# Kernel tuning notes

Hardware: AMD Instinct MI355X
Metric: run time of the kernel (lower is better)

## Reference

```python
import jax, jax.numpy as jnp
import numpy as np

N_ATOMS = 100000
N_BONDS = 200000
N_MOLS = 4000
ATOMS_PER_MOL = 25
MAX_NB = 6
ATOM_FDIM = 133
BOND_FDIM = 14
HIDDEN = 300
DEPTH = 3


def setup_inputs() -> dict:
    key = jax.random.key(0)
    ks = jax.random.split(key, 8)
    f_atoms = jax.random.normal(ks[0], (N_ATOMS, ATOM_FDIM), dtype=jnp.float32)
    f_bonds = jax.random.normal(ks[1], (N_BONDS, BOND_FDIM), dtype=jnp.float32)
    # incoming-bond lists per atom (irregular gather targets)
    a2b = jax.random.randint(ks[2], (N_ATOMS, MAX_NB), 0, N_BONDS, dtype=jnp.int32)
    # source atom of each directed bond
    b2a = jax.random.randint(ks[3], (N_BONDS,), 0, N_ATOMS, dtype=jnp.int32)
    # reverse bond: directed bonds come in pairs (2i, 2i+1)
    b2revb = (jnp.arange(N_BONDS, dtype=jnp.int32) ^ 1)
    # contiguous [start, size] per molecule
    starts = jnp.arange(N_MOLS, dtype=jnp.int32) * ATOMS_PER_MOL
    sizes = jnp.full((N_MOLS,), ATOMS_PER_MOL, dtype=jnp.int32)
    a_scope = jnp.stack([starts, sizes], axis=1)
    W_i = jax.random.normal(ks[4], (HIDDEN, ATOM_FDIM + BOND_FDIM), dtype=jnp.float32) * 0.05
    W_h = jax.random.normal(ks[5], (HIDDEN, HIDDEN), dtype=jnp.float32) * 0.05
    W_o = jax.random.normal(ks[6], (HIDDEN, ATOM_FDIM + HIDDEN), dtype=jnp.float32) * 0.05
    b_o = jax.random.normal(ks[7], (HIDDEN,), dtype=jnp.float32) * 0.05
    return {"f_atoms": f_atoms, "f_bonds": f_bonds, "a2b": a2b, "b2a": b2a,
            "b2revb": b2revb, "a_scope": a_scope, "W_i": W_i, "W_h": W_h,
            "W_o": W_o, "b_o": b_o}


def reference(f_atoms, f_bonds, a2b, b2a, b2revb, a_scope, W_i, W_h, W_o, b_o):
    # initial directed-bond messages: [f_atoms[src], f_bonds] -> Linear -> ReLU
    input_feats = jnp.concatenate([f_atoms[b2a], f_bonds], axis=1)  # (E, 147)
    message = jax.nn.relu(input_feats @ W_i.T)  # (E, H)
    for _ in range(DEPTH - 1):
        nei_a_message = message[a2b].sum(axis=1)          # (V, H) gather+sum
        nei_message = nei_a_message[b2a] - message[b2revb]  # (E, H)
        message = jax.nn.relu(nei_message @ W_h.T)
    a_message = message[a2b].sum(axis=1)  # (V, H)
    atom_hiddens = jax.nn.relu(jnp.concatenate([f_atoms, a_message], axis=1) @ W_o.T + b_o)
    # vectorized scope mean-pool (scopes are contiguous ranges)
    starts = a_scope[:, 0]
    sizes = a_scope[:, 1]
    seg_ids = jnp.searchsorted(starts, jnp.arange(atom_hiddens.shape[0]), side='right') - 1
    sums = jax.ops.segment_sum(atom_hiddens, seg_ids, num_segments=N_MOLS)
    denom = jnp.maximum(sizes, 1).astype(atom_hiddens.dtype)[:, None]
    mol_vecs = jnp.where((sizes > 0)[:, None], sums / denom, 0.0)
    return mol_vecs
```

## Files before the change

### kernel.cpp

```cpp
#include <hip/hip_runtime.h>
#include <stdint.h>

#define N_ATOMS   100000
#define N_BONDS   200000
#define N_MOLS    4000
#define MAX_NB    6
#define ATOM_FDIM 133
#define BOND_FDIM 14
#define HIDDEN    300
#define NPAD      320

typedef __attribute__((ext_vector_type(8))) short          bf16x8;
typedef __attribute__((ext_vector_type(8))) unsigned short u16x8;
typedef __attribute__((ext_vector_type(4))) float          f32x4;
typedef __attribute__((ext_vector_type(4))) unsigned int   u32x4;

static __device__ __forceinline__ float u2f(unsigned int u) {
  union { unsigned int u; float f; } v; v.u = u; return v.f;
}
static __device__ __forceinline__ unsigned int f2u(float f) {
  union { float f; unsigned int u; } v; v.f = f; return v.u;
}
static __device__ __forceinline__ float bflo(unsigned int u) { return u2f(u << 16); }
static __device__ __forceinline__ float bfhi(unsigned int u) { return u2f(u & 0xffff0000u); }
static __device__ __forceinline__ unsigned short f2bf_rn(float f) {
  unsigned int u = f2u(f);
  return (unsigned short)((u + 0x7fffu + ((u >> 16) & 1u)) >> 16);
}
static __device__ __forceinline__ unsigned int pack_rn(float lo, float hi) {
  return ((unsigned int)f2bf_rn(hi) << 16) | f2bf_rn(lo);
}

__global__ __launch_bounds__(256) void convw_kernel(
    const float* __restrict__ w, unsigned short* __restrict__ o,
    int Ksrc, int seg1, int src2off, int seg2dst, int seg2len, int KP) {
  int total = NPAD * KP;
  for (int idx = blockIdx.x * 256 + threadIdx.x; idx < total; idx += gridDim.x * 256) {
    int n = idx / KP, k = idx - n * KP;
    int src = -1;
    if (k < seg1) src = k;
    else if (k >= seg2dst && k < seg2dst + seg2len) src = src2off + (k - seg2dst);
    float v = (n < HIDDEN && src >= 0) ? w[(size_t)n * Ksrc + src] : 0.f;
    o[idx] = f2bf_rn(v);
  }
}

template<int KP, int MODE, int FS, int FW, bool RELU, bool BIAS>
__global__ __launch_bounds__(256, 2) void gemm_dense(
    const float* __restrict__ Af, const unsigned short* Ab,
    const unsigned short* __restrict__ W, const float* __restrict__ bias,
    unsigned short* out, int M) {
  constexpr int NST = KP / 32;
  __shared__ __align__(16) unsigned short As[NST * 2048];

  const int b0   = blockIdx.x * 64;
  const int tid  = threadIdx.x;
  const int lane = tid & 63;
  const int wave = tid >> 6;
  const int sr   = tid >> 2;
  const int q    = tid & 3;

  int row = b0 + sr;
  if (row >= M) row = M - 1;
  const int dbase = (sr >> 4) * 512 + (q * 16 + (sr & 15)) * 8;

  auto stage_chunk = [&](int ks) -> u16x8 {
    u16x8 r;
    if (MODE == 0) {
      r = *(const u16x8*)(Ab + (size_t)row * KP + ks * 32 + q * 8);
    } else if (MODE == 1) {
#pragma unroll
      for (int j = 0; j < 8; j++) {
        int k = ks * 32 + q * 8 + j;
        float v = (k < FW) ? Af[(size_t)row * FS + k] : 0.f;
        r[j] = f2bf_rn(v);
      }
    } else {
      if (ks < 5) {
#pragma unroll
        for (int j = 0; j < 8; j++) {
          int k = ks * 32 + q * 8 + j;
          float v = (k < ATOM_FDIM) ? Af[(size_t)row * ATOM_FDIM + k] : 0.f;
          r[j] = f2bf_rn(v);
        }
      } else {
        r = *(const u16x8*)(Ab + (size_t)row * NPAD + (ks - 5) * 32 + q * 8);
      }
    }
    return r;
  };

  constexpr int G = (NST < 5) ? NST : 5;
#pragma unroll
  for (int ks0 = 0; ks0 < NST; ks0 += G) {
    u16x8 vals[G];
#pragma unroll
    for (int j = 0; j < G; j++) { int ks = ks0 + j; if (ks < NST) vals[j] = stage_chunk(ks); }
#pragma unroll
    for (int j = 0; j < G; j++) { int ks = ks0 + j; if (ks < NST) *(u16x8*)&As[ks * 2048 + dbase] = vals[j]; }
  }
  __syncthreads();

  f32x4 acc[4][5];
#pragma unroll
  for (int m = 0; m < 4; m++)
#pragma unroll
    for (int n = 0; n < 5; n++) acc[m][n] = (f32x4){0.f, 0.f, 0.f, 0.f};

  const int nbase = wave * 80;
  const int ar = lane & 15, kq = lane >> 4;
  const unsigned short* Wl = W + (size_t)(nbase + ar) * KP + kq * 8;

#pragma unroll
  for (int ks = 0; ks < NST; ks++) {
    bf16x8 af[4];
#pragma unroll
    for (int m = 0; m < 4; m++) af[m] = *(const bf16x8*)&As[ks * 2048 + m * 512 + lane * 8];
#pragma unroll
    for (int nf = 0; nf < 5; nf++) {
      bf16x8 bfr = *(const bf16x8*)(Wl + (size_t)nf * 16 * KP + ks * 32);
#pragma unroll
      for (int m = 0; m < 4; m++)
        acc[m][nf] = __builtin_amdgcn_mfma_f32_16x16x32_bf16(af[m], bfr, acc[m][nf], 0, 0, 0);
    }
  }

#pragma unroll
  for (int m = 0; m < 4; m++) {
#pragma unroll
    for (int rr = 0; rr < 4; rr++) {
      int orow = b0 + m * 16 + (lane >> 4) * 4 + rr;
      if (orow >= M) continue;
#pragma unroll
      for (int nf = 0; nf < 5; nf++) {
        int ocol = nbase + nf * 16 + ar;
        float v = acc[m][nf][rr];
        if (BIAS) v += (ocol < HIDDEN) ? bias[ocol] : 0.f;
        if (RELU) v = v > 0.f ? v : 0.f;
        out[(size_t)orow * NPAD + ocol] = f2bf_rn(v);
      }
    }
  }
}

__global__ __launch_bounds__(256) void agg_kernel(
    const unsigned short* __restrict__ src, const int* __restrict__ a2b,
    unsigned short* __restrict__ dst) {
  const int TPA = NPAD / 16;
  int idx = blockIdx.x * 256 + threadIdx.x;
  if (idx >= N_ATOMS * TPA) return;
  int a  = idx / TPA;
  int kc = (idx - a * TPA) * 16;
  int bidx[MAX_NB];
#pragma unroll
  for (int j = 0; j < MAX_NB; j++) bidx[j] = a2b[a * MAX_NB + j];
  float slo[8], shi[8];
#pragma unroll
  for (int t = 0; t < 8; t++) { slo[t] = 0.f; shi[t] = 0.f; }
#pragma unroll
  for (int j = 0; j < MAX_NB; j++) {
    const u32x4* p = (const u32x4*)(src + (size_t)bidx[j] * NPAD + kc);
    u32x4 v0 = p[0], v1 = p[1];
#pragma unroll
    for (int t = 0; t < 4; t++) {
      slo[t]     += bflo(v0[t]); shi[t]     += bfhi(v0[t]);
      slo[4 + t] += bflo(v1[t]); shi[4 + t] += bfhi(v1[t]);
    }
  }
  u32x4 o0, o1;
#pragma unroll
  for (int t = 0; t < 4; t++) { o0[t] = pack_rn(slo[t], shi[t]); o1[t] = pack_rn(slo[4 + t], shi[4 + t]); }
  u32x4* qp = (u32x4*)(dst + (size_t)a * NPAD + kc);
  qp[0] = o0; qp[1] = o1;
}

__global__ __launch_bounds__(256) void combine0_kernel(
    const unsigned short* __restrict__ PAi, const unsigned short* PBi,
    const int* __restrict__ b2a, unsigned short* msg) {
  const int TPB = NPAD / 16;
  int idx = blockIdx.x * 256 + threadIdx.x;
  if (idx >= N_BONDS * TPB) return;
  int b  = idx / TPB;
  int kc = (idx - b * TPB) * 16;
  int g = b2a[b];
  const u32x4* pa = (const u32x4*)(PAi + (size_t)g * NPAD + kc);
  const u32x4* pb = (const u32x4*)(PBi + (size_t)b * NPAD + kc);
  u32x4 a0 = pa[0], a1 = pa[1], b0 = pb[0], b1 = pb[1];
  u32x4 o0, o1;
#pragma unroll
  for (int t = 0; t < 4; t++) {
    float l0 = bflo(a0[t]) + bflo(b0[t]), h0 = bfhi(a0[t]) + bfhi(b0[t]);
    float l1 = bflo(a1[t]) + bflo(b1[t]), h1 = bfhi(a1[t]) + bfhi(b1[t]);
    l0 = l0 > 0.f ? l0 : 0.f; h0 = h0 > 0.f ? h0 : 0.f;
    l1 = l1 > 0.f ? l1 : 0.f; h1 = h1 > 0.f ? h1 : 0.f;
    o0[t] = pack_rn(l0, h0); o1[t] = pack_rn(l1, h1);
  }
  u32x4* qp = (u32x4*)(msg + (size_t)b * NPAD + kc);
  qp[0] = o0; qp[1] = o1;
}

__global__ __launch_bounds__(256) void combineH_kernel(
    const unsigned short* __restrict__ neiZ, const unsigned short* Zh,
    const int* __restrict__ b2a, unsigned short* msg) {
  const int TPB = NPAD / 16;
  const int NPAIR = N_BONDS / 2;
  int idx = blockIdx.x * 256 + threadIdx.x;
  if (idx >= NPAIR * TPB) return;
  int p  = idx / TPB;
  int kc = (idx - p * TPB) * 16;
  int b0i = 2 * p, b1i = 2 * p + 1;
  int g0 = b2a[b0i], g1 = b2a[b1i];
  const u32x4* pn0 = (const u32x4*)(neiZ + (size_t)g0 * NPAD + kc);
  const u32x4* pn1 = (const u32x4*)(neiZ + (size_t)g1 * NPAD + kc);
  const u32x4* pz0 = (const u32x4*)(Zh + (size_t)b1i * NPAD + kc);
  const u32x4* pz1 = (const u32x4*)(Zh + (size_t)b0i * NPAD + kc);
  u32x4 n00 = pn0[0], n01 = pn0[1], n10 = pn1[0], n11 = pn1[1];
  u32x4 z00 = pz0[0], z01 = pz0[1], z10 = pz1[0], z11 = pz1[1];
  u32x4 o00, o01, o10, o11;
#pragma unroll
  for (int t = 0; t < 4; t++) {
    float a, c;
    a = bflo(n00[t]) - bflo(z00[t]); c = bfhi(n00[t]) - bfhi(z00[t]);
    o00[t] = pack_rn(a > 0.f ? a : 0.f, c > 0.f ? c : 0.f);
    a = bflo(n01[t]) - bflo(z01[t]); c = bfhi(n01[t]) - bfhi(z01[t]);
    o01[t] = pack_rn(a > 0.f ? a : 0.f, c > 0.f ? c : 0.f);
    a = bflo(n10[t]) - bflo(z10[t]); c = bfhi(n10[t]) - bfhi(z10[t]);
    o10[t] = pack_rn(a > 0.f ? a : 0.f, c > 0.f ? c : 0.f);
    a = bflo(n11[t]) - bflo(z11[t]); c = bfhi(n11[t]) - bfhi(z11[t]);
    o11[t] = pack_rn(a > 0.f ? a : 0.f, c > 0.f ? c : 0.f);
  }
  u32x4* q0 = (u32x4*)(msg + (size_t)b0i * NPAD + kc);
  u32x4* q1 = (u32x4*)(msg + (size_t)b1i * NPAD + kc);
  q0[0] = o00; q0[1] = o01; q1[0] = o10; q1[1] = o11;
}

__global__ __launch_bounds__(256) void readout_kernel(
    const unsigned short* __restrict__ hidden, const int* __restrict__ a_scope,
    float* __restrict__ out) {
  const int TPM = NPAD / 8;
  int idx = blockIdx.x * 256 + threadIdx.x;
  if (idx >= N_MOLS * TPM) return;
  int m = idx / TPM;
  int c = (idx - m * TPM) * 8;
  int start = a_scope[m * 2], size = a_scope[m * 2 + 1];
  float s[8];
#pragma unroll
  for (int t = 0; t < 8; t++) s[t] = 0.f;
  for (int i = 0; i < size; i++) {
    const u32x4 v = *(const u32x4*)(hidden + (size_t)(start + i) * NPAD + c);
#pragma unroll
    for (int t = 0; t < 4; t++) { s[2 * t] += bflo(v[t]); s[2 * t + 1] += bfhi(v[t]); }
  }
  float inv = (size > 0) ? 1.f / (float)size : 0.f;
#pragma unroll
  for (int t = 0; t < 8; t++) {
    int col = c + t;
    if (col < HIDDEN) out[(size_t)m * HIDDEN + col] = s[t] * inv;
  }
}

extern "C" void kernel_launch(void* const* d_in, const int* in_sizes, int n_in,
                              void* d_out, int out_size, void* d_ws, size_t ws_size,
                              hipStream_t stream) {
  const float* f_atoms = (const float*)d_in[0];
  const float* f_bonds = (const float*)d_in[1];
  const int*   a2b     = (const int*)d_in[2];
  const int*   b2a     = (const int*)d_in[3];
  const int*   a_scope = (const int*)d_in[5];
  const float* W_i     = (const float*)d_in[6];
  const float* W_h     = (const float*)d_in[7];
  const float* W_o     = (const float*)d_in[8];
  const float* b_o     = (const float*)d_in[9];
  float* out = (float*)d_out;

  char* ws = (char*)d_ws;
  size_t off = 0;
  auto alloc = [&](size_t bytes) { size_t o = off; off += (bytes + 255) & ~(size_t)255; return o; };
  unsigned short* msg  = (unsigned short*)(ws + alloc((size_t)N_BONDS * NPAD * 2));
  unsigned short* bufC = (unsigned short*)(ws + alloc((size_t)N_ATOMS * NPAD * 2));
  unsigned short* WiA  = (unsigned short*)(ws + alloc((size_t)NPAD * 160 * 2));
  unsigned short* WiB  = (unsigned short*)(ws + alloc((size_t)NPAD * 32 * 2));
  unsigned short* Wh   = (unsigned short*)(ws + alloc((size_t)NPAD * 320 * 2));
  unsigned short* Wo   = (unsigned short*)(ws + alloc((size_t)NPAD * 480 * 2));

  convw_kernel<<<(NPAD * 160 + 255) / 256, 256, 0, stream>>>(W_i, WiA, 147, 133, 0, 0, 0, 160);
  convw_kernel<<<(NPAD * 32 + 255) / 256, 256, 0, stream>>>(W_i, WiB, 147, 0, 133, 0, 14, 32);
  convw_kernel<<<(NPAD * 320 + 255) / 256, 256, 0, stream>>>(W_h, Wh, 300, 300, 0, 0, 0, 320);
  convw_kernel<<<(NPAD * 480 + 255) / 256, 256, 0, stream>>>(W_o, Wo, 433, 133, 133, 160, 300, 480);

  const int ga = (N_ATOMS + 63) / 64;
  const int gb = N_BONDS / 64;
  const int gagg = (N_ATOMS * (NPAD / 16) + 255) / 256;
  const int gcmb = (N_BONDS * (NPAD / 16) + 255) / 256;
  const int gpar = ((N_BONDS / 2) * (NPAD / 16) + 255) / 256;

  unsigned short* PAi = bufC;
  unsigned short* PBi = msg;
  unsigned short* Zh  = msg;
  unsigned short* neiZ = bufC;
  unsigned short* amsg = bufC;
  unsigned short* hidden = bufC;

  gemm_dense<160, 1, ATOM_FDIM, ATOM_FDIM, false, false><<<ga, 256, 0, stream>>>(
      f_atoms, nullptr, WiA, nullptr, PAi, N_ATOMS);
  gemm_dense<32, 1, BOND_FDIM, BOND_FDIM, false, false><<<gb, 256, 0, stream>>>(
      f_bonds, nullptr, WiB, nullptr, PBi, N_BONDS);
  combine0_kernel<<<gcmb, 256, 0, stream>>>(PAi, PBi, b2a, msg);

  for (int d = 0; d < 2; d++) {
    gemm_dense<320, 0, 0, 0, false, false><<<gb, 256, 0, stream>>>(
        nullptr, msg, Wh, nullptr, Zh, N_BONDS);
    agg_kernel<<<gagg, 256, 0, stream>>>(Zh, a2b, neiZ);
    combineH_kernel<<<gpar, 256, 0, stream>>>(neiZ, Zh, b2a, msg);
  }

  agg_kernel<<<gagg, 256, 0, stream>>>(msg, a2b, amsg);
  gemm_dense<480, 2, 0, 0, true, true><<<ga, 256, 0, stream>>>(
      f_atoms, amsg, Wo, b_o, hidden, N_ATOMS);
  readout_kernel<<<(N_MOLS * (NPAD / 8) + 255) / 256, 256, 0, stream>>>(hidden, a_scope, out);
}
```

Measured before the change: 798.7 us.

## Load GEMM A-fragments directly from global memory instead of staging in LDS

Measured after the change: 900.2 us. +12.7%, slower.

```diff
diff --git a/kernel.cpp b/kernel.cpp
--- a/kernel.cpp
+++ b/kernel.cpp
@@ -45,77 +45,62 @@
   }
 }
 
-template<int KP, int MODE, int FS, int FW, bool RELU, bool BIAS>
-__global__ __launch_bounds__(256, 2) void gemm_dense(
+template<int KP, int MODE, int FS, int FW, bool RELU, bool BIAS, bool SYNC>
+__global__ __launch_bounds__(256) void gemm_direct(
     const float* __restrict__ Af, const unsigned short* Ab,
     const unsigned short* __restrict__ W, const float* __restrict__ bias,
     unsigned short* out, int M) {
   constexpr int NST = KP / 32;
-  __shared__ __align__(16) unsigned short As[NST * 2048];
-
   const int b0   = blockIdx.x * 64;
-  const int tid  = threadIdx.x;
-  const int lane = tid & 63;
-  const int wave = tid >> 6;
-  const int sr   = tid >> 2;
-  const int q    = tid & 3;
-
-  int row = b0 + sr;
-  if (row >= M) row = M - 1;
-  const int dbase = (sr >> 4) * 512 + (q * 16 + (sr & 15)) * 8;
-
-  auto stage_chunk = [&](int ks) -> u16x8 {
-    u16x8 r;
+  const int lane = threadIdx.x & 63;
+  const int wave = threadIdx.x >> 6;
+  const int ar   = lane & 15;
+  const int kq   = lane >> 4;
+
+  int rowm[4];
+#pragma unroll
+  for (int m = 0; m < 4; m++) {
+    int row = b0 + m * 16 + ar;
+    rowm[m] = (row < M) ? row : (M - 1);
+  }
+
+  f32x4 acc[4][5];
+#pragma unroll
+  for (int m = 0; m < 4; m++)
+#pragma unroll
+    for (int n = 0; n < 5; n++) acc[m][n] = (f32x4){0.f, 0.f, 0.f, 0.f};
+
+  const int nbase = wave * 80;
+  const unsigned short* Wl = W + (size_t)(nbase + ar) * KP + kq * 8;
+
+  auto load_afrag = [&](int m, int ks) -> bf16x8 {
+    union { u32x4 u; bf16x8 h; } cv;
     if (MODE == 0) {
-      r = *(const u16x8*)(Ab + (size_t)row * KP + ks * 32 + q * 8);
-    } else if (MODE == 1) {
-#pragma unroll
-      for (int j = 0; j < 8; j++) {
-        int k = ks * 32 + q * 8 + j;
-        float v = (k < FW) ? Af[(size_t)row * FS + k] : 0.f;
-        r[j] = f2bf_rn(v);
-      }
-    } else {
-      if (ks < 5) {
-#pragma unroll
-        for (int j = 0; j < 8; j++) {
-          int k = ks * 32 + q * 8 + j;
-          float v = (k < ATOM_FDIM) ? Af[(size_t)row * ATOM_FDIM + k] : 0.f;
-          r[j] = f2bf_rn(v);
-        }
-      } else {
-        r = *(const u16x8*)(Ab + (size_t)row * NPAD + (ks - 5) * 32 + q * 8);
-      }
-    }
-    return r;
+      cv.u = *(const u32x4*)(Ab + (size_t)rowm[m] * KP + ks * 32 + kq * 8);
+      return cv.h;
+    }
+    if (MODE == 2 && ks >= 5) {
+      cv.u = *(const u32x4*)(Ab + (size_t)rowm[m] * NPAD + (ks - 5) * 32 + kq * 8);
+      return cv.h;
+    }
+    constexpr int fs = (MODE == 2) ? ATOM_FDIM : FS;
+    constexpr int fw = (MODE == 2) ? ATOM_FDIM : FW;
+    float v[8];
+#pragma unroll
+    for (int j = 0; j < 8; j++) {
+      int k = ks * 32 + kq * 8 + j;
+      v[j] = (k < fw) ? Af[(size_t)rowm[m] * fs + k] : 0.f;
+    }
+    cv.u[0] = pack_rn(v[0], v[1]); cv.u[1] = pack_rn(v[2], v[3]);
+    cv.u[2] = pack_rn(v[4], v[5]); cv.u[3] = pack_rn(v[6], v[7]);
+    return cv.h;
   };
-
-  constexpr int G = (NST < 5) ? NST : 5;
-#pragma unroll
-  for (int ks0 = 0; ks0 < NST; ks0 += G) {
-    u16x8 vals[G];
-#pragma unroll
-    for (int j = 0; j < G; j++) { int ks = ks0 + j; if (ks < NST) vals[j] = stage_chunk(ks); }
-#pragma unroll
-    for (int j = 0; j < G; j++) { int ks = ks0 + j; if (ks < NST) *(u16x8*)&As[ks * 2048 + dbase] = vals[j]; }
-  }
-  __syncthreads();
-
-  f32x4 acc[4][5];
-#pragma unroll
-  for (int m = 0; m < 4; m++)
-#pragma unroll
-    for (int n = 0; n < 5; n++) acc[m][n] = (f32x4){0.f, 0.f, 0.f, 0.f};
-
-  const int nbase = wave * 80;
-  const int ar = lane & 15, kq = lane >> 4;
-  const unsigned short* Wl = W + (size_t)(nbase + ar) * KP + kq * 8;
 
 #pragma unroll
   for (int ks = 0; ks < NST; ks++) {
     bf16x8 af[4];
 #pragma unroll
-    for (int m = 0; m < 4; m++) af[m] = *(const bf16x8*)&As[ks * 2048 + m * 512 + lane * 8];
+    for (int m = 0; m < 4; m++) af[m] = load_afrag(m, ks);
 #pragma unroll
     for (int nf = 0; nf < 5; nf++) {
       bf16x8 bfr = *(const bf16x8*)(Wl + (size_t)nf * 16 * KP + ks * 32);
@@ -125,11 +110,13 @@
     }
   }
 
+  if (SYNC) __syncthreads();
+
 #pragma unroll
   for (int m = 0; m < 4; m++) {
 #pragma unroll
     for (int rr = 0; rr < 4; rr++) {
-      int orow = b0 + m * 16 + (lane >> 4) * 4 + rr;
+      int orow = b0 + m * 16 + kq * 4 + rr;
       if (orow >= M) continue;
 #pragma unroll
       for (int nf = 0; nf < 5; nf++) {
@@ -301,21 +288,21 @@
   unsigned short* amsg = bufC;
   unsigned short* hidden = bufC;
 
-  gemm_dense<160, 1, ATOM_FDIM, ATOM_FDIM, false, false><<<ga, 256, 0, stream>>>(
+  gemm_direct<160, 1, ATOM_FDIM, ATOM_FDIM, false, false, false><<<ga, 256, 0, stream>>>(
       f_atoms, nullptr, WiA, nullptr, PAi, N_ATOMS);
-  gemm_dense<32, 1, BOND_FDIM, BOND_FDIM, false, false><<<gb, 256, 0, stream>>>(
+  gemm_direct<32, 1, BOND_FDIM, BOND_FDIM, false, false, false><<<gb, 256, 0, stream>>>(
       f_bonds, nullptr, WiB, nullptr, PBi, N_BONDS);
   combine0_kernel<<<gcmb, 256, 0, stream>>>(PAi, PBi, b2a, msg);
 
   for (int d = 0; d < 2; d++) {
-    gemm_dense<320, 0, 0, 0, false, false><<<gb, 256, 0, stream>>>(
+    gemm_direct<320, 0, 0, 0, false, false, true><<<gb, 256, 0, stream>>>(
         nullptr, msg, Wh, nullptr, Zh, N_BONDS);
     agg_kernel<<<gagg, 256, 0, stream>>>(Zh, a2b, neiZ);
     combineH_kernel<<<gpar, 256, 0, stream>>>(neiZ, Zh, b2a, msg);
   }
 
   agg_kernel<<<gagg, 256, 0, stream>>>(msg, a2b, amsg);
-  gemm_dense<480, 2, 0, 0, true, true><<<ga, 256, 0, stream>>>(
+  gemm_direct<480, 2, ATOM_FDIM, ATOM_FDIM, true, true, true><<<ga, 256, 0, stream>>>(
       f_atoms, amsg, Wo, b_o, hidden, N_ATOMS);
   readout_kernel<<<(N_MOLS * (NPAD / 8) + 255) / 256, 256, 0, stream>>>(hidden, a_scope, out);
 }
```

## Fuse bond-message combine steps into GEMM A-tile staging and prefetch weight fragments

Applied to the files above, without the earlier changes.

Measured after the change: 723.1 us. 1.1x faster.

```diff
diff --git a/kernel.cpp b/kernel.cpp
--- a/kernel.cpp
+++ b/kernel.cpp
@@ -45,11 +45,12 @@
   }
 }
 
-template<int KP, int MODE, int FS, int FW, bool RELU, bool BIAS>
-__global__ __launch_bounds__(256, 2) void gemm_dense(
-    const float* __restrict__ Af, const unsigned short* Ab,
-    const unsigned short* __restrict__ W, const float* __restrict__ bias,
-    unsigned short* out, int M) {
+template<int KP, int SRC, bool RELU, bool BIAS>
+__global__ __launch_bounds__(256, 2) void gemm_bp(
+    const float* __restrict__ Af, const float* __restrict__ F2,
+    const unsigned short* Ab, const unsigned short* __restrict__ Nei,
+    const int* __restrict__ gmap, const unsigned short* __restrict__ W,
+    const float* __restrict__ bias, unsigned short* out, int M) {
   constexpr int NST = KP / 32;
   __shared__ __align__(16) unsigned short As[NST * 2048];
 
@@ -62,29 +63,44 @@
 
   int row = b0 + sr;
   if (row >= M) row = M - 1;
+  int g = 0;
+  if (SRC == 0 || SRC == 3) g = gmap[row];
+  const int rev = row ^ 1;
   const int dbase = (sr >> 4) * 512 + (q * 16 + (sr & 15)) * 8;
 
   auto stage_chunk = [&](int ks) -> u16x8 {
+    const int kc = ks * 32 + q * 8;
     u16x8 r;
-    if (MODE == 0) {
-      r = *(const u16x8*)(Ab + (size_t)row * KP + ks * 32 + q * 8);
-    } else if (MODE == 1) {
+    if (SRC == 1) {
+      r = *(const u16x8*)(Ab + (size_t)row * KP + kc);
+    } else if (SRC == 3) {
+      u16x8 n8 = *(const u16x8*)(Nei + (size_t)g * NPAD + kc);
+      u16x8 z8 = *(const u16x8*)(Ab + (size_t)rev * NPAD + kc);
+#pragma unroll
+      for (int j = 0; j < 8; j += 2) {
+        unsigned int nu = ((const unsigned int*)&n8)[j >> 1];
+        unsigned int zu = ((const unsigned int*)&z8)[j >> 1];
+        float lo = bflo(nu) - bflo(zu), hi = bfhi(nu) - bfhi(zu);
+        lo = lo > 0.f ? lo : 0.f; hi = hi > 0.f ? hi : 0.f;
+        ((unsigned int*)&r)[j >> 1] = pack_rn(lo, hi);
+      }
+    } else if (SRC == 0) {
 #pragma unroll
       for (int j = 0; j < 8; j++) {
-        int k = ks * 32 + q * 8 + j;
-        float v = (k < FW) ? Af[(size_t)row * FS + k] : 0.f;
+        int k = kc + j; float v = 0.f;
+        if (k < ATOM_FDIM) v = Af[(size_t)g * ATOM_FDIM + k];
+        else if (k >= 160 && k < 160 + BOND_FDIM) v = F2[(size_t)row * BOND_FDIM + (k - 160)];
         r[j] = f2bf_rn(v);
       }
     } else {
-      if (ks < 5) {
+      if (kc >= 160) {
+        r = *(const u16x8*)(Ab + (size_t)row * NPAD + (kc - 160));
+      } else {
 #pragma unroll
         for (int j = 0; j < 8; j++) {
-          int k = ks * 32 + q * 8 + j;
-          float v = (k < ATOM_FDIM) ? Af[(size_t)row * ATOM_FDIM + k] : 0.f;
-          r[j] = f2bf_rn(v);
+          int k = kc + j;
+          r[j] = (k < ATOM_FDIM) ? f2bf_rn(Af[(size_t)row * ATOM_FDIM + k]) : (unsigned short)0;
         }
-      } else {
-        r = *(const u16x8*)(Ab + (size_t)row * NPAD + (ks - 5) * 32 + q * 8);
       }
     }
     return r;
@@ -111,25 +127,35 @@
   const int ar = lane & 15, kq = lane >> 4;
   const unsigned short* Wl = W + (size_t)(nbase + ar) * KP + kq * 8;
 
+  bf16x8 bnxt[5];
+#pragma unroll
+  for (int nf = 0; nf < 5; nf++) bnxt[nf] = *(const bf16x8*)(Wl + (size_t)nf * 16 * KP);
+
 #pragma unroll
   for (int ks = 0; ks < NST; ks++) {
+    bf16x8 bcur[5];
+#pragma unroll
+    for (int nf = 0; nf < 5; nf++) bcur[nf] = bnxt[nf];
+    if (ks + 1 < NST) {
+#pragma unroll
+      for (int nf = 0; nf < 5; nf++)
+        bnxt[nf] = *(const bf16x8*)(Wl + (size_t)nf * 16 * KP + (ks + 1) * 32);
+    }
     bf16x8 af[4];
 #pragma unroll
     for (int m = 0; m < 4; m++) af[m] = *(const bf16x8*)&As[ks * 2048 + m * 512 + lane * 8];
 #pragma unroll
-    for (int nf = 0; nf < 5; nf++) {
-      bf16x8 bfr = *(const bf16x8*)(Wl + (size_t)nf * 16 * KP + ks * 32);
+    for (int nf = 0; nf < 5; nf++)
 #pragma unroll
       for (int m = 0; m < 4; m++)
-        acc[m][nf] = __builtin_amdgcn_mfma_f32_16x16x32_bf16(af[m], bfr, acc[m][nf], 0, 0, 0);
-    }
+        acc[m][nf] = __builtin_amdgcn_mfma_f32_16x16x32_bf16(af[m], bcur[nf], acc[m][nf], 0, 0, 0);
   }
 
 #pragma unroll
   for (int m = 0; m < 4; m++) {
 #pragma unroll
     for (int rr = 0; rr < 4; rr++) {
-      int orow = b0 + m * 16 + (lane >> 4) * 4 + rr;
+      int orow = b0 + m * 16 + kq * 4 + rr;
       if (orow >= M) continue;
 #pragma unroll
       for (int nf = 0; nf < 5; nf++) {
@@ -171,31 +197,6 @@
 #pragma unroll
   for (int t = 0; t < 4; t++) { o0[t] = pack_rn(slo[t], shi[t]); o1[t] = pack_rn(slo[4 + t], shi[4 + t]); }
   u32x4* qp = (u32x4*)(dst + (size_t)a * NPAD + kc);
-  qp[0] = o0; qp[1] = o1;
-}
-
-__global__ __launch_bounds__(256) void combine0_kernel(
-    const unsigned short* __restrict__ PAi, const unsigned short* PBi,
-    const int* __restrict__ b2a, unsigned short* msg) {
-  const int TPB = NPAD / 16;
-  int idx = blockIdx.x * 256 + threadIdx.x;
-  if (idx >= N_BONDS * TPB) return;
-  int b  = idx / TPB;
-  int kc = (idx - b * TPB) * 16;
-  int g = b2a[b];
-  const u32x4* pa = (const u32x4*)(PAi + (size_t)g * NPAD + kc);
-  const u32x4* pb = (const u32x4*)(PBi + (size_t)b * NPAD + kc);
-  u32x4 a0 = pa[0], a1 = pa[1], b0 = pb[0], b1 = pb[1];
-  u32x4 o0, o1;
-#pragma unroll
-  for (int t = 0; t < 4; t++) {
-    float l0 = bflo(a0[t]) + bflo(b0[t]), h0 = bfhi(a0[t]) + bfhi(b0[t]);
-    float l1 = bflo(a1[t]) + bflo(b1[t]), h1 = bfhi(a1[t]) + bfhi(b1[t]);
-    l0 = l0 > 0.f ? l0 : 0.f; h0 = h0 > 0.f ? h0 : 0.f;
-    l1 = l1 > 0.f ? l1 : 0.f; h1 = h1 > 0.f ? h1 : 0.f;
-    o0[t] = pack_rn(l0, h0); o1[t] = pack_rn(l1, h1);
-  }
-  u32x4* qp = (u32x4*)(msg + (size_t)b * NPAD + kc);
   qp[0] = o0; qp[1] = o1;
 }
 
@@ -276,46 +277,38 @@
   char* ws = (char*)d_ws;
   size_t off = 0;
   auto alloc = [&](size_t bytes) { size_t o = off; off += (bytes + 255) & ~(size_t)255; return o; };
-  unsigned short* msg  = (unsigned short*)(ws + alloc((size_t)N_BONDS * NPAD * 2));
-  unsigned short* bufC = (unsigned short*)(ws + alloc((size_t)N_ATOMS * NPAD * 2));
-  unsigned short* WiA  = (unsigned short*)(ws + alloc((size_t)NPAD * 160 * 2));
-  unsigned short* WiB  = (unsigned short*)(ws + alloc((size_t)NPAD * 32 * 2));
+  unsigned short* P    = (unsigned short*)(ws + alloc((size_t)N_BONDS * NPAD * 2));
+  unsigned short* Q    = (unsigned short*)(ws + alloc((size_t)N_BONDS * NPAD * 2));
+  unsigned short* WiAB = (unsigned short*)(ws + alloc((size_t)NPAD * 192 * 2));
   unsigned short* Wh   = (unsigned short*)(ws + alloc((size_t)NPAD * 320 * 2));
   unsigned short* Wo   = (unsigned short*)(ws + alloc((size_t)NPAD * 480 * 2));
 
-  convw_kernel<<<(NPAD * 160 + 255) / 256, 256, 0, stream>>>(W_i, WiA, 147, 133, 0, 0, 0, 160);
-  convw_kernel<<<(NPAD * 32 + 255) / 256, 256, 0, stream>>>(W_i, WiB, 147, 0, 133, 0, 14, 32);
+  convw_kernel<<<(NPAD * 192 + 255) / 256, 256, 0, stream>>>(W_i, WiAB, 147, 133, 133, 160, 14, 192);
   convw_kernel<<<(NPAD * 320 + 255) / 256, 256, 0, stream>>>(W_h, Wh, 300, 300, 0, 0, 0, 320);
   convw_kernel<<<(NPAD * 480 + 255) / 256, 256, 0, stream>>>(W_o, Wo, 433, 133, 133, 160, 300, 480);
 
-  const int ga = (N_ATOMS + 63) / 64;
-  const int gb = N_BONDS / 64;
+  const int gridB = (N_BONDS + 63) / 64;
+  const int gridA = (N_ATOMS + 63) / 64;
   const int gagg = (N_ATOMS * (NPAD / 16) + 255) / 256;
-  const int gcmb = (N_BONDS * (NPAD / 16) + 255) / 256;
   const int gpar = ((N_BONDS / 2) * (NPAD / 16) + 255) / 256;
 
-  unsigned short* PAi = bufC;
-  unsigned short* PBi = msg;
-  unsigned short* Zh  = msg;
-  unsigned short* neiZ = bufC;
-  unsigned short* amsg = bufC;
-  unsigned short* hidden = bufC;
-
-  gemm_dense<160, 1, ATOM_FDIM, ATOM_FDIM, false, false><<<ga, 256, 0, stream>>>(
-      f_atoms, nullptr, WiA, nullptr, PAi, N_ATOMS);
-  gemm_dense<32, 1, BOND_FDIM, BOND_FDIM, false, false><<<gb, 256, 0, stream>>>(
-      f_bonds, nullptr, WiB, nullptr, PBi, N_BONDS);
-  combine0_kernel<<<gcmb, 256, 0, stream>>>(PAi, PBi, b2a, msg);
-
-  for (int d = 0; d < 2; d++) {
-    gemm_dense<320, 0, 0, 0, false, false><<<gb, 256, 0, stream>>>(
-        nullptr, msg, Wh, nullptr, Zh, N_BONDS);
-    agg_kernel<<<gagg, 256, 0, stream>>>(Zh, a2b, neiZ);
-    combineH_kernel<<<gpar, 256, 0, stream>>>(neiZ, Zh, b2a, msg);
-  }
-
-  agg_kernel<<<gagg, 256, 0, stream>>>(msg, a2b, amsg);
-  gemm_dense<480, 2, 0, 0, true, true><<<ga, 256, 0, stream>>>(
-      f_atoms, amsg, Wo, b_o, hidden, N_ATOMS);
-  readout_kernel<<<(N_MOLS * (NPAD / 8) + 255) / 256, 256, 0, stream>>>(hidden, a_scope, out);
-}
+  gemm_bp<192, 0, true, false><<<gridB, 256, 0, stream>>>(
+      f_atoms, f_bonds, nullptr, nullptr, b2a, WiAB, nullptr, P, N_BONDS);
+
+  gemm_bp<320, 1, false, false><<<gridB, 256, 0, stream>>>(
+      nullptr, nullptr, P, nullptr, nullptr, Wh, nullptr, Q, N_BONDS);
+
+  agg_kernel<<<gagg, 256, 0, stream>>>(Q, a2b, P);
+
+  gemm_bp<320, 3, false, false><<<gridB, 256, 0, stream>>>(
+      nullptr, nullptr, Q, P, b2a, Wh, nullptr, Q, N_BONDS);
+
+  agg_kernel<<<gagg, 256, 0, stream>>>(Q, a2b, P);
+  combineH_kernel<<<gpar, 256, 0, stream>>>(P, Q, b2a, Q);
+
+  agg_kernel<<<gagg, 256, 0, stream>>>(Q, a2b, P);
+  gemm_bp<480, 2, true, true><<<gridA, 256, 0, stream>>>(
+      f_atoms, nullptr, P, nullptr, nullptr, Wo, b_o, Q, N_ATOMS);
+
+  readout_kernel<<<(N_MOLS * (NPAD / 8) + 255) / 256, 256, 0, stream>>>(Q, a_scope, out);
+}
```
